# Kernel tuning notes

Measured on AMD Instinct MI355X. Metric: run time of the kernel, lower is better.

Reference implementation:

```python
import jax, jax.numpy as jnp
import numpy as np

N = 50000
E = 500000
H = 128


def _linear(x, w, b):
    # torch nn.Linear: y = x @ W.T + b, W is [out, in]
    return x @ w.T + b


def _layer(x, h, edge_index, w0_w, w0_b, wl_w, wl_b, w1_w, w1_b):
    # PyG MessagePassing(aggr='add', flow='target_to_source'):
    # x_j = h[edge_index[1]], scatter-add into edge_index[0], dim_size = N
    msg = h[edge_index[1]]                               # [E, H] gather
    aggr = jax.ops.segment_sum(msg, edge_index[0], num_segments=h.shape[0])  # [N, H]
    return _linear(aggr, wl_w, wl_b) + _linear(h, w0_w, w0_b) + _linear(x, w1_w, w1_b)


def setup_inputs() -> dict:
    key = jax.random.key(0)
    ks = jax.random.split(key, 12)
    wscale = 0.05
    return {
        "x_a": jax.random.normal(ks[0], (N, H), jnp.float32),
        "x_b": jax.random.normal(ks[1], (N, H), jnp.float32),
        "edge_ab": jax.random.randint(ks[2], (2, E), 0, N, jnp.int32),
        "edge_ba": jax.random.randint(ks[3], (2, E), 0, N, jnp.int32),
        "conv0_w0_w": jax.random.normal(ks[4], (H, H), jnp.float32) * wscale,
        "conv0_w0_b": jnp.zeros((H,), jnp.float32),
        "conv0_wl_w": jax.random.normal(ks[5], (H, H), jnp.float32) * wscale,
        "conv0_wl_b": jnp.zeros((H,), jnp.float32),
        "conv0_w1_w": jax.random.normal(ks[6], (H, H), jnp.float32) * wscale,
        "conv0_w1_b": jnp.zeros((H,), jnp.float32),
        "conv1_w0_w": jax.random.normal(ks[7], (H, H), jnp.float32) * wscale,
        "conv1_w0_b": jnp.zeros((H,), jnp.float32),
        "conv1_wl_w": jax.random.normal(ks[8], (H, H), jnp.float32) * wscale,
        "conv1_wl_b": jnp.zeros((H,), jnp.float32),
        "conv1_w1_w": jax.random.normal(ks[9], (H, H), jnp.float32) * wscale,
        "conv1_w1_b": jnp.zeros((H,), jnp.float32),
        "out_w": jax.random.normal(ks[10], (H, H), jnp.float32) * wscale,
        "out_b": jnp.zeros((H,), jnp.float32),
    }


def reference(x_a, x_b, edge_ab, edge_ba,
              conv0_w0_w, conv0_w0_b, conv0_wl_w, conv0_wl_b, conv0_w1_w, conv0_w1_b,
              conv1_w0_w, conv1_w0_b, conv1_wl_w, conv1_wl_b, conv1_w1_w, conv1_w1_b,
              out_w, out_b):
    # metapath = [(a, r1, b), (b, r2, a)], loop over reversed(metapath):
    # iter 0: conv_idx=1, edge (b, r2, a), dst='a'
    h_a = jax.nn.relu(_layer(x_a, x_a, edge_ba,
                             conv1_w0_w, conv1_w0_b, conv1_wl_w, conv1_wl_b, conv1_w1_w, conv1_w1_b))
    # iter 1: conv_idx=0, edge (a, r1, b), dst='b'
    h_b = jax.nn.relu(_layer(x_b, x_b, edge_ab,
                             conv0_w0_w, conv0_w0_b, conv0_wl_w, conv0_wl_b, conv0_w1_w, conv0_w1_b))
    # start_type = 'a'
    return _linear(h_a, out_w, out_b)
```

## Files before the change

### kernel.cpp

```cpp
#include <hip/hip_runtime.h>
#include <hip/hip_bf16.h>

#define NN 50000
#define NE 500000
#define HD 128
#define CAP 128
#define PREP_B 24
#define PREPX_B 3125
#define ZAGGR_B 6250
#define ZCUR_B ((NN + 255) / 256)
#define SETUP_B (PREP_B + PREPX_B + ZAGGR_B + ZCUR_B)

typedef __bf16 bf16;
typedef __attribute__((ext_vector_type(8))) __bf16 bf16x8;
typedef __attribute__((ext_vector_type(4))) float floatx4;

__device__ inline float u2f(unsigned int lo16) {
    union { unsigned int i; float f; } c; c.i = lo16 << 16; return c.f;
}

__device__ inline bf16x8 cvt8(floatx4 a, floatx4 b) {
    bf16x8 r;
#pragma unroll
    for (int j = 0; j < 4; j++) { r[j] = (bf16)a[j]; r[j + 4] = (bf16)b[j]; }
    return r;
}

__device__ inline void split8(const floatx4 f0, const floatx4 f1, bf16x8& hi, bf16x8& lo) {
#pragma unroll
    for (int j = 0; j < 4; j++) {
        float a = f0[j]; bf16 h = (bf16)a; hi[j] = h; lo[j] = (bf16)(a - (float)h);
        float b = f1[j]; bf16 g = (bf16)b; hi[j + 4] = g; lo[j + 4] = (bf16)(b - (float)g);
    }
}

__device__ inline bf16x8 zero8() {
    bf16x8 v;
#pragma unroll
    for (int j = 0; j < 8; j++) v[j] = (bf16)0.f;
    return v;
}

__global__ __launch_bounds__(256) void k_setup(
    const float* __restrict__ wl, const float* __restrict__ w0, const float* __restrict__ w1,
    const float* __restrict__ bl, const float* __restrict__ b0, const float* __restrict__ b1,
    const float* __restrict__ ow, const float* __restrict__ ob,
    const float* __restrict__ x,
    bf16* __restrict__ wlb, bf16* __restrict__ w01b, bf16* __restrict__ owb,
    float* __restrict__ bias1, float* __restrict__ bias2,
    bf16* __restrict__ xb, float* __restrict__ aggr, int* __restrict__ cur,
    int tier)
{
    const int b = blockIdx.x, tid = threadIdx.x;
    if (b < PREP_B) {
        int g = b * 256 + tid;
        int m = g >> 11, off = (g & 2047) << 3;
        if (m == 0) {
            const floatx4 a = *(const floatx4*)(wl + off);
            const floatx4 c = *(const floatx4*)(wl + off + 4);
            *(bf16x8*)(wlb + off) = cvt8(a, c);
        } else if (m == 1) {
            floatx4 a = *(const floatx4*)(w0 + off);
            floatx4 c = *(const floatx4*)(w0 + off + 4);
            const floatx4 d = *(const floatx4*)(w1 + off);
            const floatx4 e = *(const floatx4*)(w1 + off + 4);
#pragma unroll
            for (int j = 0; j < 4; j++) { a[j] += d[j]; c[j] += e[j]; }
            *(bf16x8*)(w01b + off) = cvt8(a, c);
        } else {
            const floatx4 a = *(const floatx4*)(ow + off);
            const floatx4 c = *(const floatx4*)(ow + off + 4);
            *(bf16x8*)(owb + off) = cvt8(a, c);
        }
        if (g < 128) bias1[g] = bl[g] + b0[g] + b1[g];
        else if (g < 256) bias2[g - 128] = ob[g - 128];
    } else if (b < PREP_B + PREPX_B) {
        if (tier >= 1) {
            int off = ((b - PREP_B) * 256 + tid) << 3;
            const floatx4 a = *(const floatx4*)(x + off);
            const floatx4 c = *(const floatx4*)(x + off + 4);
            *(bf16x8*)(xb + off) = cvt8(a, c);
        }
    } else if (b < PREP_B + PREPX_B + ZAGGR_B) {
        int i = (b - PREP_B - PREPX_B) * 256 + tid;
        floatx4 z = {0.f, 0.f, 0.f, 0.f};
        ((floatx4*)aggr)[i] = z;
    } else {
        if (tier >= 1) {
            int i = (b - PREP_B - PREPX_B - ZAGGR_B) * 256 + tid;
            if (i < NN) cur[i] = 0;
        }
    }
}

__global__ __launch_bounds__(256) void k_fillb(const int* __restrict__ edge,
                                               const float* __restrict__ x,
                                               int* __restrict__ cur,
                                               int* __restrict__ bucket,
                                               float* __restrict__ aggr) {
    int e = blockIdx.x * 256 + threadIdx.x;
    if (e >= NE) return;
    int dst = edge[e];
    int src = edge[NE + e];
    int pos = atomicAdd(&cur[dst], 1);
    if (pos < CAP) {
        bucket[dst * CAP + pos] = src;
    } else {
        const float* xr = x + (size_t)src * HD;
        float* ar = aggr + (size_t)dst * HD;
        for (int c = 0; c < HD; c++) unsafeAtomicAdd(ar + c, xr[c]);
    }
}

__global__ __launch_bounds__(256) void k_aggr(const unsigned int* __restrict__ xb2,
                                              const int* __restrict__ cur,
                                              const int* __restrict__ bucket,
                                              float* __restrict__ aggr) {
    int w = (blockIdx.x * 256 + threadIdx.x) >> 6;
    int lane = threadIdx.x & 63;
    if (w >= NN) return;
    int deg = cur[w];
    int n = (deg < CAP) ? deg : CAP;
    const int* bk = bucket + w * CAP;
    float ax = 0.f, ay = 0.f;
    if (deg > CAP) {
        float2 init = ((float2*)aggr)[(size_t)w * 64 + lane];
        ax = init.x; ay = init.y;
    }
    int d = 0;
    for (; d + 3 < n; d += 4) {
        int s0 = bk[d], s1 = bk[d + 1], s2 = bk[d + 2], s3 = bk[d + 3];
        unsigned int v0 = xb2[s0 * 64 + lane];
        unsigned int v1 = xb2[s1 * 64 + lane];
        unsigned int v2 = xb2[s2 * 64 + lane];
        unsigned int v3 = xb2[s3 * 64 + lane];
        ax += u2f(v0 & 0xffff) + u2f(v1 & 0xffff) + u2f(v2 & 0xffff) + u2f(v3 & 0xffff);
        ay += u2f(v0 >> 16) + u2f(v1 >> 16) + u2f(v2 >> 16) + u2f(v3 >> 16);
    }
    for (; d < n; d++) {
        unsigned int v = xb2[bk[d] * 64 + lane];
        ax += u2f(v & 0xffff); ay += u2f(v >> 16);
    }
    float2 o; o.x = ax; o.y = ay;
    ((float2*)aggr)[(size_t)w * 64 + lane] = o;
}

__global__ __launch_bounds__(256) void k_scatter(const float* __restrict__ x,
                                                 const int* __restrict__ edge,
                                                 float* __restrict__ aggr) {
    int tid = blockIdx.x * 256 + threadIdx.x;
    int e = tid >> 5;
    int c = (tid & 31) << 2;
    int dst = edge[e];
    int src = edge[NE + e];
    const floatx4 v = *(const floatx4*)(x + src * HD + c);
    float* ap = aggr + dst * HD + c;
    unsafeAtomicAdd(ap + 0, v[0]);
    unsafeAtomicAdd(ap + 1, v[1]);
    unsafeAtomicAdd(ap + 2, v[2]);
    unsafeAtomicAdd(ap + 3, v[3]);
}

__global__ __launch_bounds__(256) void k_gemm12(
    const float* __restrict__ aggr, const float* __restrict__ x, const bf16* __restrict__ xb,
    int use_xb,
    const bf16* __restrict__ wlb, const bf16* __restrict__ w01b, const bf16* __restrict__ owb,
    const float* __restrict__ bias1, const float* __restrict__ bias2,
    float* __restrict__ out)
{
    __shared__ bf16 sA[128 * 136];
    __shared__ bf16 sB[128 * 136];
    __shared__ float b1_s[128], b2_s[128];
    float* tp = (float*)sB;
    const int tid = threadIdx.x;

#pragma unroll
    for (int it = 0; it < 8; it++) {
        int i = tid + it * 256;
        int r = i >> 4;
        int o = (i & 15) << 3;
        *(bf16x8*)(sA + r * 136 + o) = *(const bf16x8*)(wlb  + r * 128 + o);
        *(bf16x8*)(sB + r * 136 + o) = *(const bf16x8*)(w01b + r * 128 + o);
    }
    if (tid < 128) { b1_s[tid] = bias1[tid]; b2_s[tid] = bias2[tid]; }
    __syncthreads();

    const int lane = tid & 63;
    const int wv   = tid >> 6;
    const int ln   = lane & 15;
    const int quad = lane >> 4;
    const int row0 = blockIdx.x * 64 + wv * 16;
    const int arow = row0 + ln;
    const bool aok = arow < NN;

    floatx4 acc[8] = {};

#pragma unroll
    for (int kc = 0; kc < 4; kc++) {
        const int k0 = kc * 32 + quad * 8;
        bf16x8 a_hi = zero8(), a_lo = zero8(), a_x = zero8();
        if (aok) {
            const floatx4 f0 = *(const floatx4*)(aggr + arow * 128 + k0);
            const floatx4 f1 = *(const floatx4*)(aggr + arow * 128 + k0 + 4);
            split8(f0, f1, a_hi, a_lo);
            if (use_xb) {
                a_x = *(const bf16x8*)(xb + arow * 128 + k0);
            } else {
                const floatx4 g0 = *(const floatx4*)(x + arow * 128 + k0);
                const floatx4 g1 = *(const floatx4*)(x + arow * 128 + k0 + 4);
                a_x = cvt8(g0, g1);
            }
        }
#pragma unroll
        for (int nc = 0; nc < 8; nc++) {
            const bf16x8 bw  = *(const bf16x8*)(sA + (nc * 16 + ln) * 136 + k0);
            const bf16x8 bw2 = *(const bf16x8*)(sB + (nc * 16 + ln) * 136 + k0);
            acc[nc] = __builtin_amdgcn_mfma_f32_16x16x32_bf16(a_hi, bw,  acc[nc], 0, 0, 0);
            acc[nc] = __builtin_amdgcn_mfma_f32_16x16x32_bf16(a_lo, bw,  acc[nc], 0, 0, 0);
            acc[nc] = __builtin_amdgcn_mfma_f32_16x16x32_bf16(a_x,  bw2, acc[nc], 0, 0, 0);
        }
    }
    __syncthreads();

#pragma unroll
    for (int it = 0; it < 8; it++) {
        int i = tid + it * 256;
        int r = i >> 4;
        int o = (i & 15) << 3;
        *(bf16x8*)(sA + r * 136 + o) = *(const bf16x8*)(owb + r * 128 + o);
    }
#pragma unroll
    for (int nc = 0; nc < 8; nc++) {
        const int col = nc * 16 + ln;
        const float bv = b1_s[col];
#pragma unroll
        for (int r = 0; r < 4; r++) {
            float v = acc[nc][r] + bv;
            tp[wv * 2112 + (quad * 4 + r) * 132 + col] = (v > 0.f ? v : 0.f);
        }
        acc[nc][0] = acc[nc][1] = acc[nc][2] = acc[nc][3] = 0.f;
    }
    __syncthreads();

#pragma unroll
    for (int kc = 0; kc < 4; kc++) {
        const int k0 = kc * 32 + quad * 8;
        const floatx4 f0 = *(const floatx4*)(tp + wv * 2112 + ln * 132 + k0);
        const floatx4 f1 = *(const floatx4*)(tp + wv * 2112 + ln * 132 + k0 + 4);
        bf16x8 a_hi, a_lo;
        split8(f0, f1, a_hi, a_lo);
#pragma unroll
        for (int nc = 0; nc < 8; nc++) {
            const bf16x8 bw = *(const bf16x8*)(sA + (nc * 16 + ln) * 136 + k0);
            acc[nc] = __builtin_amdgcn_mfma_f32_16x16x32_bf16(a_hi, bw, acc[nc], 0, 0, 0);
            acc[nc] = __builtin_amdgcn_mfma_f32_16x16x32_bf16(a_lo, bw, acc[nc], 0, 0, 0);
        }
    }

#pragma unroll
    for (int nc = 0; nc < 8; nc++) {
        const int col = nc * 16 + ln;
        const float bv = b2_s[col];
#pragma unroll
        for (int r = 0; r < 4; r++) {
            const int row = row0 + quad * 4 + r;
            if (row < NN) out[row * 128 + col] = acc[nc][r] + bv;
        }
    }
}

extern "C" void kernel_launch(void* const* d_in, const int* in_sizes, int n_in,
                              void* d_out, int out_size, void* d_ws, size_t ws_size,
                              hipStream_t stream) {
    const float* x_a     = (const float*)d_in[0];
    const int*   edge_ba = (const int*)d_in[3];
    const float* c1_w0_w = (const float*)d_in[10];
    const float* c1_w0_b = (const float*)d_in[11];
    const float* c1_wl_w = (const float*)d_in[12];
    const float* c1_wl_b = (const float*)d_in[13];
    const float* c1_w1_w = (const float*)d_in[14];
    const float* c1_w1_b = (const float*)d_in[15];
    const float* out_w   = (const float*)d_in[16];
    const float* out_b   = (const float*)d_in[17];

    char* p = (char*)d_ws;
    float* aggr  = (float*)p;   p += (size_t)NN * HD * 4;
    bf16*  wlb   = (bf16*)p;    p += 32768;
    bf16*  w01b  = (bf16*)p;    p += 32768;
    bf16*  owb   = (bf16*)p;    p += 32768;
    float* bias1 = (float*)p;   p += 512;
    float* bias2 = (float*)p;   p += 512;
    const size_t WS_FALL = (size_t)(p - (char*)d_ws);
    int*   cur    = (int*)p;    p += 200704;
    int*   bucket = (int*)p;    p += (size_t)NN * CAP * 4;
    bf16*  xb     = (bf16*)p;   p += (size_t)NN * HD * 2;
    const size_t WS_BUCKET = (size_t)(p - (char*)d_ws);

    const int tier = (ws_size >= WS_BUCKET) ? 1 : 0;

    k_setup<<<SETUP_B, 256, 0, stream>>>(c1_wl_w, c1_w0_w, c1_w1_w,
                                         c1_wl_b, c1_w0_b, c1_w1_b,
                                         out_w, out_b, x_a,
                                         wlb, w01b, owb, bias1, bias2,
                                         xb, aggr, cur, tier);

    if (tier) {
        k_fillb<<<(NE + 255) / 256, 256, 0, stream>>>(edge_ba, x_a, cur, bucket, aggr);
        k_aggr <<<(NN * 64 + 255) / 256, 256, 0, stream>>>((const unsigned int*)xb,
                                                           cur, bucket, aggr);
    } else {
        k_scatter<<<NE * 32 / 256, 256, 0, stream>>>(x_a, edge_ba, aggr);
    }

    k_gemm12<<<(NN + 63) / 64, 256, 0, stream>>>(aggr, x_a, xb, tier,
                                                 wlb, w01b, owb, bias1, bias2,
                                                 (float*)d_out);
}
```

Baseline: 200.9 us.

## Fuse x-to-bf16 conversion into bucket fill; process four nodes per wavefront in aggregation

Result: faster. 195.5 us (-2.7%).

```diff
diff --git a/kernel.cpp b/kernel.cpp
--- a/kernel.cpp
+++ b/kernel.cpp
@@ -6,10 +6,12 @@
 #define HD 128
 #define CAP 128
 #define PREP_B 24
-#define PREPX_B 3125
+#define ZCUR_B ((NN + 255) / 256)
 #define ZAGGR_B 6250
-#define ZCUR_B ((NN + 255) / 256)
-#define SETUP_B (PREP_B + PREPX_B + ZAGGR_B + ZCUR_B)
+#define K1_B (PREP_B + ZCUR_B + ZAGGR_B)
+#define FILLB_B ((NE + 255) / 256)
+#define XCONV_B 3125
+#define K2_B (FILLB_B + XCONV_B)
 
 typedef __bf16 bf16;
 typedef __attribute__((ext_vector_type(8))) __bf16 bf16x8;
@@ -41,15 +43,13 @@
     return v;
 }
 
-__global__ __launch_bounds__(256) void k_setup(
+__global__ __launch_bounds__(256) void k_setup1(
     const float* __restrict__ wl, const float* __restrict__ w0, const float* __restrict__ w1,
     const float* __restrict__ bl, const float* __restrict__ b0, const float* __restrict__ b1,
     const float* __restrict__ ow, const float* __restrict__ ob,
-    const float* __restrict__ x,
     bf16* __restrict__ wlb, bf16* __restrict__ w01b, bf16* __restrict__ owb,
     float* __restrict__ bias1, float* __restrict__ bias2,
-    bf16* __restrict__ xb, float* __restrict__ aggr, int* __restrict__ cur,
-    int tier)
+    float* __restrict__ aggr, int* __restrict__ cur, int tier)
 {
     const int b = blockIdx.x, tid = threadIdx.x;
     if (b < PREP_B) {
@@ -74,75 +74,107 @@
         }
         if (g < 128) bias1[g] = bl[g] + b0[g] + b1[g];
         else if (g < 256) bias2[g - 128] = ob[g - 128];
-    } else if (b < PREP_B + PREPX_B) {
+    } else if (b < PREP_B + ZCUR_B) {
         if (tier >= 1) {
-            int off = ((b - PREP_B) * 256 + tid) << 3;
-            const floatx4 a = *(const floatx4*)(x + off);
-            const floatx4 c = *(const floatx4*)(x + off + 4);
-            *(bf16x8*)(xb + off) = cvt8(a, c);
-        }
-    } else if (b < PREP_B + PREPX_B + ZAGGR_B) {
-        int i = (b - PREP_B - PREPX_B) * 256 + tid;
+            int i = (b - PREP_B) * 256 + tid;
+            if (i < NN) cur[i] = 0;
+        }
+    } else {
+        int i = (b - PREP_B - ZCUR_B) * 256 + tid;
         floatx4 z = {0.f, 0.f, 0.f, 0.f};
         ((floatx4*)aggr)[i] = z;
+    }
+}
+
+__global__ __launch_bounds__(256) void k_setup2(
+    const int* __restrict__ edge, const float* __restrict__ x,
+    int* __restrict__ cur, int* __restrict__ bucket, float* __restrict__ aggr,
+    bf16* __restrict__ xb)
+{
+    const int b = blockIdx.x, tid = threadIdx.x;
+    if (b < FILLB_B) {
+        int e = b * 256 + tid;
+        if (e >= NE) return;
+        int dst = edge[e];
+        int src = edge[NE + e];
+        int pos = atomicAdd(&cur[dst], 1);
+        if (pos < CAP) {
+            bucket[dst * CAP + pos] = src;
+        } else {
+            const float* xr = x + (size_t)src * HD;
+            float* ar = aggr + (size_t)dst * HD;
+            for (int c = 0; c < HD; c++) unsafeAtomicAdd(ar + c, xr[c]);
+        }
     } else {
-        if (tier >= 1) {
-            int i = (b - PREP_B - PREPX_B - ZAGGR_B) * 256 + tid;
-            if (i < NN) cur[i] = 0;
-        }
-    }
-}
-
-__global__ __launch_bounds__(256) void k_fillb(const int* __restrict__ edge,
-                                               const float* __restrict__ x,
-                                               int* __restrict__ cur,
-                                               int* __restrict__ bucket,
-                                               float* __restrict__ aggr) {
-    int e = blockIdx.x * 256 + threadIdx.x;
-    if (e >= NE) return;
-    int dst = edge[e];
-    int src = edge[NE + e];
-    int pos = atomicAdd(&cur[dst], 1);
-    if (pos < CAP) {
-        bucket[dst * CAP + pos] = src;
-    } else {
-        const float* xr = x + (size_t)src * HD;
-        float* ar = aggr + (size_t)dst * HD;
-        for (int c = 0; c < HD; c++) unsafeAtomicAdd(ar + c, xr[c]);
-    }
-}
-
-__global__ __launch_bounds__(256) void k_aggr(const unsigned int* __restrict__ xb2,
+        int off = ((b - FILLB_B) * 256 + tid) << 3;
+        const floatx4 a = *(const floatx4*)(x + off);
+        const floatx4 c = *(const floatx4*)(x + off + 4);
+        *(bf16x8*)(xb + off) = cvt8(a, c);
+    }
+}
+
+__global__ __launch_bounds__(256) void k_aggr(const bf16* __restrict__ xb,
                                               const int* __restrict__ cur,
                                               const int* __restrict__ bucket,
                                               float* __restrict__ aggr) {
-    int w = (blockIdx.x * 256 + threadIdx.x) >> 6;
-    int lane = threadIdx.x & 63;
-    if (w >= NN) return;
-    int deg = cur[w];
-    int n = (deg < CAP) ? deg : CAP;
-    const int* bk = bucket + w * CAP;
-    float ax = 0.f, ay = 0.f;
-    if (deg > CAP) {
-        float2 init = ((float2*)aggr)[(size_t)w * 64 + lane];
-        ax = init.x; ay = init.y;
-    }
-    int d = 0;
-    for (; d + 3 < n; d += 4) {
-        int s0 = bk[d], s1 = bk[d + 1], s2 = bk[d + 2], s3 = bk[d + 3];
-        unsigned int v0 = xb2[s0 * 64 + lane];
-        unsigned int v1 = xb2[s1 * 64 + lane];
-        unsigned int v2 = xb2[s2 * 64 + lane];
-        unsigned int v3 = xb2[s3 * 64 + lane];
-        ax += u2f(v0 & 0xffff) + u2f(v1 & 0xffff) + u2f(v2 & 0xffff) + u2f(v3 & 0xffff);
-        ay += u2f(v0 >> 16) + u2f(v1 >> 16) + u2f(v2 >> 16) + u2f(v3 >> 16);
-    }
-    for (; d < n; d++) {
-        unsigned int v = xb2[bk[d] * 64 + lane];
-        ax += u2f(v & 0xffff); ay += u2f(v >> 16);
-    }
-    float2 o; o.x = ax; o.y = ay;
-    ((float2*)aggr)[(size_t)w * 64 + lane] = o;
+    const int gw   = (blockIdx.x * 256 + threadIdx.x) >> 6;
+    const int lane = threadIdx.x & 63;
+    const int quad = lane >> 4;
+    const int ln   = lane & 15;
+    const int node = gw * 4 + quad;
+    const bool ok  = node < NN;
+
+    float acc[8] = {0.f, 0.f, 0.f, 0.f, 0.f, 0.f, 0.f, 0.f};
+    int deg = 0, n = 0;
+    const int* bk = bucket;
+    if (ok) {
+        deg = cur[node];
+        n = (deg < CAP) ? deg : CAP;
+        bk = bucket + node * CAP;
+        if (deg > CAP) {
+            const floatx4 s0 = *(const floatx4*)(aggr + node * HD + ln * 8);
+            const floatx4 s1 = *(const floatx4*)(aggr + node * HD + ln * 8 + 4);
+#pragma unroll
+            for (int j = 0; j < 4; j++) { acc[j] = s0[j]; acc[4 + j] = s1[j]; }
+        }
+    }
+
+    int t = 0;
+    for (; t + 3 < n; t += 4) {
+        int s0 = bk[t], s1 = bk[t + 1], s2 = bk[t + 2], s3 = bk[t + 3];
+        const uint4 v0 = *(const uint4*)(xb + s0 * HD + ln * 8);
+        const uint4 v1 = *(const uint4*)(xb + s1 * HD + ln * 8);
+        const uint4 v2 = *(const uint4*)(xb + s2 * HD + ln * 8);
+        const uint4 v3 = *(const uint4*)(xb + s3 * HD + ln * 8);
+        const unsigned int u0[4] = {v0.x, v0.y, v0.z, v0.w};
+        const unsigned int u1[4] = {v1.x, v1.y, v1.z, v1.w};
+        const unsigned int u2[4] = {v2.x, v2.y, v2.z, v2.w};
+        const unsigned int u3[4] = {v3.x, v3.y, v3.z, v3.w};
+#pragma unroll
+        for (int j = 0; j < 4; j++) {
+            acc[2 * j]     += u2f(u0[j] & 0xffff) + u2f(u1[j] & 0xffff)
+                            + u2f(u2[j] & 0xffff) + u2f(u3[j] & 0xffff);
+            acc[2 * j + 1] += u2f(u0[j] >> 16) + u2f(u1[j] >> 16)
+                            + u2f(u2[j] >> 16) + u2f(u3[j] >> 16);
+        }
+    }
+    for (; t < n; t++) {
+        const uint4 v = *(const uint4*)(xb + bk[t] * HD + ln * 8);
+        const unsigned int u[4] = {v.x, v.y, v.z, v.w};
+#pragma unroll
+        for (int j = 0; j < 4; j++) {
+            acc[2 * j]     += u2f(u[j] & 0xffff);
+            acc[2 * j + 1] += u2f(u[j] >> 16);
+        }
+    }
+
+    if (ok) {
+        floatx4 o0, o1;
+#pragma unroll
+        for (int j = 0; j < 4; j++) { o0[j] = acc[j]; o1[j] = acc[4 + j]; }
+        *(floatx4*)(aggr + node * HD + ln * 8) = o0;
+        *(floatx4*)(aggr + node * HD + ln * 8 + 4) = o1;
+    }
 }
 
 __global__ __launch_bounds__(256) void k_scatter(const float* __restrict__ x,
@@ -298,16 +330,15 @@
 
     const int tier = (ws_size >= WS_BUCKET) ? 1 : 0;
 
-    k_setup<<<SETUP_B, 256, 0, stream>>>(c1_wl_w, c1_w0_w, c1_w1_w,
-                                         c1_wl_b, c1_w0_b, c1_w1_b,
-                                         out_w, out_b, x_a,
-                                         wlb, w01b, owb, bias1, bias2,
-                                         xb, aggr, cur, tier);
+    k_setup1<<<K1_B, 256, 0, stream>>>(c1_wl_w, c1_w0_w, c1_w1_w,
+                                       c1_wl_b, c1_w0_b, c1_w1_b,
+                                       out_w, out_b,
+                                       wlb, w01b, owb, bias1, bias2,
+                                       aggr, cur, tier);
 
     if (tier) {
-        k_fillb<<<(NE + 255) / 256, 256, 0, stream>>>(edge_ba, x_a, cur, bucket, aggr);
-        k_aggr <<<(NN * 64 + 255) / 256, 256, 0, stream>>>((const unsigned int*)xb,
-                                                           cur, bucket, aggr);
+        k_setup2<<<K2_B, 256, 0, stream>>>(edge_ba, x_a, cur, bucket, aggr, xb);
+        k_aggr  <<<3125, 256, 0, stream>>>(xb, cur, bucket, aggr);
     } else {
         k_scatter<<<NE * 32 / 256, 256, 0, stream>>>(x_a, edge_ba, aggr);
     }
```
